# Optimization experiments

Measured on AMD Instinct MI355X. Metric: run time of the kernel, lower is better.

Reference implementation:

```python
import jax, jax.numpy as jnp
import numpy as np

N_WIN = 7  # winsize in PSF.forward
EMBED_DIM = 3
N_EMBED = 8192

def _box_sum(x, n=N_WIN):
    # sliding-window sum with zero padding == torch ZeroPad2d + unfold sum
    C = x.shape[1]
    k = jnp.ones((C, 1, n, n), x.dtype)
    return jax.lax.conv_general_dilated(
        x, k, (1, 1), [(n // 2, n // 2)] * 2,
        feature_group_count=C, dimension_numbers=('NCHW', 'OIHW', 'NCHW'))

def _patch_stats(x, n=N_WIN):
    # mean / unbiased var over the n*n window (zeros included, matching unfold of zero-padded input)
    N = n * n
    s1 = _box_sum(x, n)
    s2 = _box_sum(x * x, n)
    mean = s1 / N
    var = (s2 - s1 * s1 / N) / (N - 1)  # torch .var default unbiased=True
    return mean, var

def _patch_mv_norm(x, n=N_WIN):
    m, v = _patch_stats(x, n)
    return (x - m) / (jnp.sqrt(v) + 1e-8)

def _conv1x1(x, w, b):
    return jnp.einsum('oi,bihw->bohw', w, x) + b[None, :, None, None]

def _ln(x, g, b, eps=1e-5):
    m = x.mean(-1, keepdims=True)
    v = x.var(-1, keepdims=True)
    return (x - m) / jnp.sqrt(v + eps) * g + b

def _mlp(x, w1, b1, w2, b2):
    h = jax.nn.gelu(x @ w1.T + b1, approximate=True)  # GELU(approximate='tanh')
    return h @ w2.T + b2

def _psf(front, back, e_w, e_b, f_w, f_b, g_w, g_b, h_w, h_b):
    x_norm = _patch_mv_norm(front)
    y_mean, y_var = _patch_stats(back)
    x_adain = x_norm * jnp.sqrt(y_var) + y_mean  # patch_adain (no eps on y_std)
    EE = _conv1x1(x_adain, e_w, e_b)
    FF = _conv1x1(_patch_mv_norm(front), f_w, f_b)
    GG = _conv1x1(_patch_mv_norm(back), g_w, g_b)
    HH = _conv1x1(back, h_w, h_b)
    b, c, h, w = GG.shape
    FFf = FF.reshape(b, c, h * w)
    GGf = GG.reshape(b, c, h * w)
    F_n = jnp.sqrt((FFf * FFf).sum(1))
    G_n = jnp.sqrt((GGf * GGf).sum(1))
    S = (FFf * GGf).sum(1) / (F_n * G_n)          # [b, h*w] cosine similarity
    S_min = S.min(1, keepdims=True)
    S_max = S.max(1, keepdims=True)
    S_n = ((S - S_min) / (S_max - S_min)).reshape(b, 1, h, w)
    return S_n * EE + (1 - S_n) * HH

def reference(front, back, mask, bg_embed,
              mi_w1, mi_b1, mi_w2, mi_b2,
              q_w, k_w, v_w,
              mo_w1, mo_b1, mo_w2, mo_b2,
              n1_g, n1_b, n2_g, n2_b,
              e_w, e_b, f_w, f_b, g_w, g_b, h_w, h_b,
              fuse_w, fuse_b):
    fused = _psf(front, back, e_w, e_b, f_w, f_b, g_w, g_b, h_w, h_b)  # [B,3,H,W]
    B, C, H, W = front.shape
    x = front.reshape(B, C, H * W).transpose(0, 2, 1)   # [B, HW, 3] pixel tokens
    x = _mlp(x, mi_w1, mi_b1, mi_w2, mi_b2)             # mlp_in: 3 -> 6 -> embed_dim
    x = _ln(x, n1_g, n1_b)                              # norm1
    ctx = bg_embed.T                                    # [n_embed, embed_dim] codebook as context
    q = x @ q_w.T                                       # [B, HW, d]
    k = ctx @ k_w.T                                     # [n_embed, d]
    v = ctx @ v_w.T                                     # [n_embed, d]
    scale = q.shape[-1] ** (-0.5)
    attn = jax.nn.softmax(jnp.einsum('bld,nd->bln', q, k) * scale, axis=-1)
    x = jnp.einsum('bln,nd->bld', attn, v)              # [B, HW, d]
    x = _mlp(x, mo_w1, mo_b1, mo_w2, mo_b2)             # mlp_out: d -> 6 -> 3
    x = _ln(x, n2_g, n2_b)                              # norm2
    attn_img = x.transpose(0, 2, 1).reshape(B, 3, H, W)
    out = _conv1x1(jnp.concatenate([attn_img, fused], 1), fuse_w, fuse_b)  # fuse: 6 -> 3
    return out

def setup_inputs() -> dict:
    key = jax.random.key(0)
    ks = jax.random.split(key, 32)
    B, H, W = 2, 96, 96
    d = EMBED_DIM
    n = lambda k, s: jax.random.normal(k, s, dtype=jnp.float32)
    inp = {
        'front': n(ks[0], (B, 3, H, W)),
        'back':  n(ks[1], (B, 3, H, W)),
        'mask':  jax.random.uniform(ks[2], (B, 1, H, W), dtype=jnp.float32),
        'bg_embed': n(ks[3], (d, N_EMBED)),
        'mi_w1': n(ks[4], (6, 3)) * 0.5, 'mi_b1': jnp.zeros((6,)),
        'mi_w2': n(ks[5], (d, 6)) * 0.5, 'mi_b2': jnp.zeros((d,)),
        'q_w': n(ks[6], (d, d)) * 0.5,
        'k_w': n(ks[7], (d, d)) * 0.5,
        'v_w': n(ks[8], (d, d)) * 0.5,
        'mo_w1': n(ks[9], (6, d)) * 0.5, 'mo_b1': jnp.zeros((6,)),
        'mo_w2': n(ks[10], (3, 6)) * 0.5, 'mo_b2': jnp.zeros((3,)),
        'n1_g': jnp.ones((d,)), 'n1_b': jnp.zeros((d,)),
        'n2_g': jnp.ones((3,)), 'n2_b': jnp.zeros((3,)),
        'e_w': n(ks[11], (3, 3)) * 0.3, 'e_b': jnp.zeros((3,)),
        'f_w': n(ks[12], (3, 3)) * 0.3, 'f_b': jnp.zeros((3,)),
        'g_w': n(ks[13], (3, 3)) * 0.3, 'g_b': jnp.zeros((3,)),
        'h_w': n(ks[14], (3, 3)) * 0.3, 'h_b': jnp.zeros((3,)),
        'fuse_w': n(ks[15], (3, 6)) * 0.3, 'fuse_b': jnp.zeros((3,)),
    }
    return inp
```

## Files before the change

### kernel.cpp

```cpp
#include <hip/hip_runtime.h>
#include <math.h>

#define HW    9216
#define NPIX  18432
#define NKEY  8192

#define OFF_QPK  0
#define OFF_KPK  (OFF_QPK + NPIX*8)
#define OFF_VT   (OFF_KPK + NKEY*8)
#define OFF_EEHS (OFF_VT + NKEY*4)
#define OFF_MM   (OFF_EEHS + NPIX*8)
#define OFF_PART (OFF_MM + 576)

#if __has_builtin(__builtin_amdgcn_exp2f)
#define EXP2(x) __builtin_amdgcn_exp2f(x)
#else
#define EXP2(x) exp2f(x)
#endif

typedef float f32x4 __attribute__((ext_vector_type(4)));
typedef short bf16x8 __attribute__((ext_vector_type(8)));
typedef unsigned u32x4 __attribute__((ext_vector_type(4)));

__device__ __forceinline__ unsigned bf16rne(float x){
    unsigned b = __builtin_bit_cast(unsigned, x);
    return (b + 0x7FFFu + ((b >> 16) & 1u)) >> 16;
}
__device__ __forceinline__ float bf16tof(unsigned h){
    return __builtin_bit_cast(float, h << 16);
}

__device__ __forceinline__ float gelu_tanh(float x){
    float u = 0.7978845608028654f*(x + 0.044715f*x*x*x);
    return 0.5f*x*(1.0f + tanhf(u));
}

__global__ __launch_bounds__(256) void k1_prep(
    const float* __restrict__ front, const float* __restrict__ back,
    const float* __restrict__ bg,
    const float* __restrict__ k_w,  const float* __restrict__ v_w,
    const float* __restrict__ mi_w1, const float* __restrict__ mi_b1,
    const float* __restrict__ mi_w2, const float* __restrict__ mi_b2,
    const float* __restrict__ q_w,
    const float* __restrict__ n1_g, const float* __restrict__ n1_b,
    const float* __restrict__ e_w,  const float* __restrict__ e_b,
    const float* __restrict__ f_w,  const float* __restrict__ f_b,
    const float* __restrict__ g_w,  const float* __restrict__ g_b,
    const float* __restrict__ h_w,  const float* __restrict__ h_b,
    float* __restrict__ ws)
{
    float* ws_qpk  = ws + OFF_QPK;
    float* ws_kpk  = ws + OFF_KPK;
    float* ws_eehs = ws + OFF_EEHS;
    float* ws_mm   = ws + OFF_MM;

    __shared__ float lds[6][196];
    __shared__ float red[12][256];

    int tid = threadIdx.x;
    int bid = blockIdx.x;
    int img = bid / 144;
    int t   = bid % 144;
    int ty  = (t / 12) * 8;
    int tx  = (t % 12) * 8;

    if (bid < 32){
        int key = bid*256 + tid;
        float c0=bg[key], c1=bg[NKEY+key], c2=bg[2*NKEY+key];
        float kv3[3], vv3[3];
        #pragma unroll
        for (int i=0;i<3;i++){
            kv3[i] = k_w[i*3+0]*c0 + k_w[i*3+1]*c1 + k_w[i*3+2]*c2;
            vv3[i] = v_w[i*3+0]*c0 + v_w[i*3+1]*c1 + v_w[i*3+2]*c2;
        }
        unsigned kh[3], kl[3];
        #pragma unroll
        for (int i=0;i<3;i++){
            kh[i] = bf16rne(kv3[i]);
            kl[i] = bf16rne(kv3[i] - bf16tof(kh[i]));
        }
        unsigned u[8];
        u[0] = kh[0] | (kh[1]<<16);
        u[1] = kh[2] | (kl[0]<<16);
        u[2] = kl[1] | (kl[2]<<16);
        u[3] = kh[0] | (kh[1]<<16);
        u[4] = kh[2]; u[5]=0; u[6]=0; u[7]=0;
        f32x4* kp4 = (f32x4*)ws_kpk;
        kp4[(size_t)key*2+0] = __builtin_bit_cast(f32x4, *(const u32x4*)&u[0]);
        kp4[(size_t)key*2+1] = __builtin_bit_cast(f32x4, *(const u32x4*)&u[4]);
        ((f32x4*)(ws + OFF_VT))[key] = (f32x4){vv3[0], vv3[1], vv3[2], 0.0f};
    }

    const float* fbase = front + img*3*HW;
    const float* bbase = back  + img*3*HW;

    for (int i = tid; i < 196; i += 256){
        int hy = i / 14, hx = i - hy*14;
        int gy = ty + hy - 3, gx = tx + hx - 3;
        bool ok = ((unsigned)gy < 96u) && ((unsigned)gx < 96u);
        int off = gy*96 + gx;
        #pragma unroll
        for (int c=0;c<3;c++){
            lds[c  ][i] = ok ? fbase[c*HW+off] : 0.0f;
            lds[3+c][i] = ok ? bbase[c*HW+off] : 0.0f;
        }
    }
    __syncthreads();

    int p  = tid & 63;
    int qd = tid >> 6;
    int ly = p >> 3, lx = p & 7;

    {
        float s1f[3]={0,0,0}, s2f[3]={0,0,0}, s1b[3]={0,0,0}, s2b[3]={0,0,0};
        int r0 = qd*2;
        int nr = (qd < 3) ? 2 : 1;
        for (int rr=0; rr<nr; ++rr){
            int rb = (ly + r0 + rr)*14 + lx;
            #pragma unroll
            for (int dx=0; dx<7; ++dx){
                #pragma unroll
                for (int c=0;c<3;c++){
                    float fv = lds[c  ][rb+dx];
                    float bv = lds[3+c][rb+dx];
                    s1f[c]+=fv; s2f[c]+=fv*fv;
                    s1b[c]+=bv; s2b[c]+=bv*bv;
                }
            }
        }
        #pragma unroll
        for (int c=0;c<3;c++){
            red[c  ][tid] = s1f[c];
            red[3+c][tid] = s2f[c];
            red[6+c][tid] = s1b[c];
            red[9+c][tid] = s2b[c];
        }
    }
    __syncthreads();

    if (tid < 64){
        float s1f[3]={0,0,0}, s2f[3]={0,0,0}, s1b[3]={0,0,0}, s2b[3]={0,0,0};
        #pragma unroll
        for (int q2=0; q2<4; ++q2){
            int src = p + q2*64;
            #pragma unroll
            for (int c=0;c<3;c++){
                s1f[c] += red[c  ][src];
                s2f[c] += red[3+c][src];
                s1b[c] += red[6+c][src];
                s2b[c] += red[9+c][src];
            }
        }

        int ctr = (ly+3)*14 + (lx+3);
        int pos = (ty+ly)*96 + (tx+lx);
        int pix = img*HW + pos;

        float xnf[3], adain[3], bn[3], bval[3], fctr[3];
        #pragma unroll
        for (int c=0;c<3;c++){
            float mf = s1f[c]*(1.0f/49.0f);
            float vf = (s2f[c] - s1f[c]*s1f[c]*(1.0f/49.0f))*(1.0f/48.0f);
            float fv = lds[c][ctr];
            fctr[c] = fv;
            xnf[c] = (fv - mf)/(sqrtf(vf)+1e-8f);

            float mb = s1b[c]*(1.0f/49.0f);
            float vb = (s2b[c] - s1b[c]*s1b[c]*(1.0f/49.0f))*(1.0f/48.0f);
            float bb = lds[3+c][ctr];
            bval[c]  = bb;
            float stdb = sqrtf(vb);
            adain[c] = xnf[c]*stdb + mb;
            bn[c]    = (bb - mb)/(stdb + 1e-8f);
        }

        float EE[3], FF[3], GG[3], HHv[3];
        #pragma unroll
        for (int i=0;i<3;i++){
            EE[i]  = e_w[i*3+0]*adain[0] + e_w[i*3+1]*adain[1] + e_w[i*3+2]*adain[2] + e_b[i];
            FF[i]  = f_w[i*3+0]*xnf[0]   + f_w[i*3+1]*xnf[1]   + f_w[i*3+2]*xnf[2]   + f_b[i];
            GG[i]  = g_w[i*3+0]*bn[0]    + g_w[i*3+1]*bn[1]    + g_w[i*3+2]*bn[2]    + g_b[i];
            HHv[i] = h_w[i*3+0]*bval[0]  + h_w[i*3+1]*bval[1]  + h_w[i*3+2]*bval[2]  + h_b[i];
        }
        float num = FF[0]*GG[0]+FF[1]*GG[1]+FF[2]*GG[2];
        float fn  = sqrtf(FF[0]*FF[0]+FF[1]*FF[1]+FF[2]*FF[2]);
        float gn  = sqrtf(GG[0]*GG[0]+GG[1]*GG[1]+GG[2]*GG[2]);
        float S   = num/(fn*gn);

        float4* eehs4 = (float4*)ws_eehs;
        eehs4[pix*2+0] = make_float4(EE[0],EE[1],EE[2],S);
        eehs4[pix*2+1] = make_float4(HHv[0],HHv[1],HHv[2],0.0f);

        float mn = S, mx = S;
        #pragma unroll
        for (int off=32; off>0; off>>=1){
            mn = fminf(mn, __shfl_xor(mn, off));
            mx = fmaxf(mx, __shfl_xor(mx, off));
        }
        if (p == 0){ ws_mm[bid*2+0]=mn; ws_mm[bid*2+1]=mx; }

        float xt0 = fctr[0], xt1 = fctr[1], xt2 = fctr[2];
        float h6[6];
        #pragma unroll
        for (int i=0;i<6;i++){
            float a = mi_w1[i*3+0]*xt0 + mi_w1[i*3+1]*xt1 + mi_w1[i*3+2]*xt2 + mi_b1[i];
            h6[i] = gelu_tanh(a);
        }
        float x2[3];
        #pragma unroll
        for (int i=0;i<3;i++){
            float a = mi_b2[i];
            #pragma unroll
            for (int k=0;k<6;k++) a += mi_w2[i*6+k]*h6[k];
            x2[i]=a;
        }
        float m  = (x2[0]+x2[1]+x2[2])*(1.0f/3.0f);
        float d0 = x2[0]-m, d1 = x2[1]-m, d2 = x2[2]-m;
        float var = (d0*d0+d1*d1+d2*d2)*(1.0f/3.0f);
        float inv = 1.0f/sqrtf(var+1e-5f);
        float xn0 = d0*inv*n1_g[0]+n1_b[0];
        float xn1 = d1*inv*n1_g[1]+n1_b[1];
        float xn2 = d2*inv*n1_g[2]+n1_b[2];
        const float qs = 0.5773502691896258f * 1.4426950408889634f;
        float qv[3];
        qv[0] = (q_w[0]*xn0 + q_w[1]*xn1 + q_w[2]*xn2)*qs;
        qv[1] = (q_w[3]*xn0 + q_w[4]*xn1 + q_w[5]*xn2)*qs;
        qv[2] = (q_w[6]*xn0 + q_w[7]*xn1 + q_w[8]*xn2)*qs;

        unsigned qh[3], ql[3];
        #pragma unroll
        for (int i=0;i<3;i++){
            qh[i] = bf16rne(qv[i]);
            ql[i] = bf16rne(qv[i] - bf16tof(qh[i]));
        }
        unsigned u[8];
        u[0] = qh[0] | (qh[1]<<16);
        u[1] = qh[2] | (qh[0]<<16);
        u[2] = qh[1] | (qh[2]<<16);
        u[3] = ql[0] | (ql[1]<<16);
        u[4] = ql[2]; u[5]=0; u[6]=0; u[7]=0;
        f32x4* qp4 = (f32x4*)ws_qpk;
        qp4[(size_t)pix*2+0] = __builtin_bit_cast(f32x4, *(const u32x4*)&u[0]);
        qp4[(size_t)pix*2+1] = __builtin_bit_cast(f32x4, *(const u32x4*)&u[4]);
    }
}

#define RED4(vv, mm) { vv.x += __shfl_xor(vv.x,mm); vv.y += __shfl_xor(vv.y,mm); \
                       vv.z += __shfl_xor(vv.z,mm); vv.w += __shfl_xor(vv.w,mm); }

__global__ __launch_bounds__(256) void k2_attn(const float* __restrict__ ws)
{
    const f32x4* qpk = (const f32x4*)(ws + OFF_QPK);
    const f32x4* kpk = (const f32x4*)(ws + OFF_KPK);
    const f32x4* vt  = (const f32x4*)(ws + OFF_VT);
    f32x4* part      = (f32x4*)(ws + OFF_PART);

    __shared__ f32x4 lkp[512];
    __shared__ f32x4 lv[256];

    int tid  = threadIdx.x;
    int bid  = blockIdx.x;
    int kq   = bid & 7;
    int qg   = bid >> 3;
    int wave = tid >> 6, lane = tid & 63;
    int qtile = qg*4 + wave;
    int g = lane >> 4, col = lane & 15;

    bf16x8 afrag = {0,0,0,0,0,0,0,0};
    if (g < 2)
        afrag = __builtin_bit_cast(bf16x8, qpk[(size_t)(qtile*16 + col)*2 + g]);

    f32x4 s_ = {0,0,0,0}, a0_ = {0,0,0,0}, a1_ = {0,0,0,0}, a2_ = {0,0,0,0};

    const f32x4* kpbase = kpk + ((size_t)kq*1024)*2;
    const f32x4* vbase  = vt + kq*1024;

    for (int chunk=0; chunk<4; ++chunk){
        for (int i=tid; i<512; i+=256) lkp[i] = kpbase[chunk*512 + i];
        if (tid < 256)             lv[tid] = vbase[chunk*256 + tid];
        __syncthreads();
        #pragma unroll 4
        for (int st=0; st<16; ++st){
            bf16x8 bfrag = {0,0,0,0,0,0,0,0};
            if (g < 2)
                bfrag = __builtin_bit_cast(bf16x8, lkp[(st*16+col)*2 + g]);
            f32x4 S = __builtin_amdgcn_mfma_f32_16x16x32_bf16(afrag, bfrag, (f32x4){0,0,0,0}, 0, 0, 0);
            f32x4 v = lv[st*16+col];
            f32x4 p;
            p.x = EXP2(S.x); p.y = EXP2(S.y); p.z = EXP2(S.z); p.w = EXP2(S.w);
            s_  += p;
            a0_ += p * v.x;
            a1_ += p * v.y;
            a2_ += p * v.z;
        }
        __syncthreads();
    }

    RED4(s_, 8) RED4(a0_, 8) RED4(a1_, 8) RED4(a2_, 8)
    RED4(s_, 4) RED4(a0_, 4) RED4(a1_, 4) RED4(a2_, 4)
    RED4(s_, 2) RED4(a0_, 2) RED4(a1_, 2) RED4(a2_, 2)
    RED4(s_, 1) RED4(a0_, 1) RED4(a1_, 1) RED4(a2_, 1)

    int qbase = qtile*16 + g*4;
    f32x4* dst = part + (size_t)kq*NPIX + qbase;
    if      (col==0) dst[0] = (f32x4){s_.x, a0_.x, a1_.x, a2_.x};
    else if (col==1) dst[1] = (f32x4){s_.y, a0_.y, a1_.y, a2_.y};
    else if (col==2) dst[2] = (f32x4){s_.z, a0_.z, a1_.z, a2_.z};
    else if (col==3) dst[3] = (f32x4){s_.w, a0_.w, a1_.w, a2_.w};
}

template<int NC_T>
__global__ __launch_bounds__(256) void k3_final(
    const float* __restrict__ ws,
    const float* __restrict__ mo_w1, const float* __restrict__ mo_b1,
    const float* __restrict__ mo_w2, const float* __restrict__ mo_b2,
    const float* __restrict__ n2_g,  const float* __restrict__ n2_b,
    const float* __restrict__ fuse_w,const float* __restrict__ fuse_b,
    float* __restrict__ out)
{
    const float* ws_eehs = ws + OFF_EEHS;
    const float* ws_mm   = ws + OFF_MM;
    const float* ws_part = ws + OFF_PART;

    int tid = threadIdx.x;
    int g   = tid >> 6;
    int lp  = tid & 63;
    int pixbase = blockIdx.x*64;
    int pix = pixbase + lp;
    int b   = (pix >= HW) ? 1 : 0;

    constexpr int CPG = NC_T/4;
    float s=0.0f, a0=0.0f, a1=0.0f, a2=0.0f;
    const f32x4* part4 = (const f32x4*)ws_part;
    #pragma unroll
    for (int c=g*CPG; c<(g+1)*CPG; ++c){
        f32x4 p = part4[(size_t)c*NPIX + pix];
        s+=p.x; a0+=p.y; a1+=p.z; a2+=p.w;
    }
    __shared__ f32x4 red[256];
    red[tid] = (f32x4){s,a0,a1,a2};

    __shared__ float wmn[4], wmx[4];
    float mn = INFINITY, mx = -INFINITY;
    if (tid < 144){
        mn = ws_mm[(b*144+tid)*2+0];
        mx = ws_mm[(b*144+tid)*2+1];
    }
    #pragma unroll
    for (int off=32; off>0; off>>=1){
        mn = fminf(mn, __shfl_xor(mn, off));
        mx = fmaxf(mx, __shfl_xor(mx, off));
    }
    if ((tid & 63) == 0){ wmn[tid>>6]=mn; wmx[tid>>6]=mx; }
    __syncthreads();

    if (tid < 64){
        mn = fminf(fminf(wmn[0],wmn[1]), fminf(wmn[2],wmn[3]));
        mx = fmaxf(fmaxf(wmx[0],wmx[1]), fmaxf(wmx[2],wmx[3]));

        f32x4 p0 = red[tid], p1 = red[64+tid], p2 = red[128+tid], p3 = red[192+tid];
        s  = p0.x+p1.x+p2.x+p3.x;
        a0 = p0.y+p1.y+p2.y+p3.y;
        a1 = p0.z+p1.z+p2.z+p3.z;
        a2 = p0.w+p1.w+p2.w+p3.w;
        float invs = 1.0f/s;
        float xa0 = a0*invs, xa1 = a1*invs, xa2 = a2*invs;

        float h6[6];
        #pragma unroll
        for (int i=0;i<6;i++){
            float a = mo_w1[i*3+0]*xa0 + mo_w1[i*3+1]*xa1 + mo_w1[i*3+2]*xa2 + mo_b1[i];
            h6[i] = gelu_tanh(a);
        }
        float y[3];
        #pragma unroll
        for (int i=0;i<3;i++){
            float a = mo_b2[i];
            #pragma unroll
            for (int k=0;k<6;k++) a += mo_w2[i*6+k]*h6[k];
            y[i]=a;
        }
        float m  = (y[0]+y[1]+y[2])*(1.0f/3.0f);
        float d0 = y[0]-m, d1 = y[1]-m, d2 = y[2]-m;
        float var = (d0*d0+d1*d1+d2*d2)*(1.0f/3.0f);
        float inv = 1.0f/sqrtf(var+1e-5f);
        float t0 = d0*inv*n2_g[0]+n2_b[0];
        float t1 = d1*inv*n2_g[1]+n2_b[1];
        float t2 = d2*inv*n2_g[2]+n2_b[2];

        float4 e  = ((const float4*)ws_eehs)[pix*2+0];
        float4 hh = ((const float4*)ws_eehs)[pix*2+1];
        float Sn = (e.w - mn)/(mx - mn);
        float f0 = Sn*e.x + (1.0f-Sn)*hh.x;
        float f1 = Sn*e.y + (1.0f-Sn)*hh.y;
        float f2 = Sn*e.z + (1.0f-Sn)*hh.z;

        int pos = pix - b*HW;
        #pragma unroll
        for (int o=0;o<3;o++){
            float val = fuse_b[o]
                      + fuse_w[o*6+0]*t0 + fuse_w[o*6+1]*t1 + fuse_w[o*6+2]*t2
                      + fuse_w[o*6+3]*f0 + fuse_w[o*6+4]*f1 + fuse_w[o*6+5]*f2;
            out[(b*3+o)*HW + pos] = val;
        }
    }
}

extern "C" void kernel_launch(void* const* d_in, const int* in_sizes, int n_in,
                              void* d_out, int out_size, void* d_ws, size_t ws_size,
                              hipStream_t stream) {
    const float* front  = (const float*)d_in[0];
    const float* back   = (const float*)d_in[1];
    const float* bg     = (const float*)d_in[3];
    const float* mi_w1  = (const float*)d_in[4];
    const float* mi_b1  = (const float*)d_in[5];
    const float* mi_w2  = (const float*)d_in[6];
    const float* mi_b2  = (const float*)d_in[7];
    const float* q_w    = (const float*)d_in[8];
    const float* k_w    = (const float*)d_in[9];
    const float* v_w    = (const float*)d_in[10];
    const float* mo_w1  = (const float*)d_in[11];
    const float* mo_b1  = (const float*)d_in[12];
    const float* mo_w2  = (const float*)d_in[13];
    const float* mo_b2  = (const float*)d_in[14];
    const float* n1_g   = (const float*)d_in[15];
    const float* n1_b   = (const float*)d_in[16];
    const float* n2_g   = (const float*)d_in[17];
    const float* n2_b   = (const float*)d_in[18];
    const float* e_w    = (const float*)d_in[19];
    const float* e_b    = (const float*)d_in[20];
    const float* f_w    = (const float*)d_in[21];
    const float* f_b    = (const float*)d_in[22];
    const float* g_w    = (const float*)d_in[23];
    const float* g_b    = (const float*)d_in[24];
    const float* h_w    = (const float*)d_in[25];
    const float* h_b    = (const float*)d_in[26];
    const float* fuse_w = (const float*)d_in[27];
    const float* fuse_b = (const float*)d_in[28];

    float* ws  = (float*)d_ws;
    float* out = (float*)d_out;

    k1_prep<<<dim3(288), 256, 0, stream>>>(
        front, back, bg, k_w, v_w, mi_w1, mi_b1, mi_w2, mi_b2, q_w,
        n1_g, n1_b, e_w, e_b, f_w, f_b, g_w, g_b, h_w, h_b, ws);

    k2_attn<<<dim3(2304), 256, 0, stream>>>(ws);

    k3_final<8><<<dim3(NPIX/64), 256, 0, stream>>>(
        ws, mo_w1, mo_b1, mo_w2, mo_b2, n2_g, n2_b, fuse_w, fuse_b, out);
}
```

Baseline: 50.15 us.

## Switch attention scores to 32x32x16 MFMA with 16-way key split

The attention kernel moves from 16x16x32 bf16 MFMA, where half the K dimension was zero padding, to 32x32x16 MFMA so every lane carries useful Q/K fragment data. Each wave now handles 32 queries, and the key range is split 16 ways instead of 8, with 512 keys per block. The final combine kernel is instantiated for 16 partials to match. This uses more accumulator registers (64 floats per lane), a longer 5-step shuffle reduction, and twice as many partials written to and read back from memory.

After: 93.93 us. +87.3%, slower.

```diff
diff --git a/kernel.cpp b/kernel.cpp
--- a/kernel.cpp
+++ b/kernel.cpp
@@ -18,7 +18,8 @@
 #define EXP2(x) exp2f(x)
 #endif
 
-typedef float f32x4 __attribute__((ext_vector_type(4)));
+typedef float f32x4  __attribute__((ext_vector_type(4)));
+typedef float f32x16 __attribute__((ext_vector_type(16)));
 typedef short bf16x8 __attribute__((ext_vector_type(8)));
 typedef unsigned u32x4 __attribute__((ext_vector_type(4)));
 
@@ -245,9 +246,6 @@
     }
 }
 
-#define RED4(vv, mm) { vv.x += __shfl_xor(vv.x,mm); vv.y += __shfl_xor(vv.y,mm); \
-                       vv.z += __shfl_xor(vv.z,mm); vv.w += __shfl_xor(vv.w,mm); }
-
 __global__ __launch_bounds__(256) void k2_attn(const float* __restrict__ ws)
 {
     const f32x4* qpk = (const f32x4*)(ws + OFF_QPK);
@@ -260,53 +258,64 @@
 
     int tid  = threadIdx.x;
     int bid  = blockIdx.x;
-    int kq   = bid & 7;
-    int qg   = bid >> 3;
+    int kq   = bid & 15;
+    int qg   = bid >> 4;
     int wave = tid >> 6, lane = tid & 63;
     int qtile = qg*4 + wave;
-    int g = lane >> 4, col = lane & 15;
-
-    bf16x8 afrag = {0,0,0,0,0,0,0,0};
-    if (g < 2)
-        afrag = __builtin_bit_cast(bf16x8, qpk[(size_t)(qtile*16 + col)*2 + g]);
-
-    f32x4 s_ = {0,0,0,0}, a0_ = {0,0,0,0}, a1_ = {0,0,0,0}, a2_ = {0,0,0,0};
-
-    const f32x4* kpbase = kpk + ((size_t)kq*1024)*2;
-    const f32x4* vbase  = vt + kq*1024;
-
-    for (int chunk=0; chunk<4; ++chunk){
+    int col  = lane & 31;
+    int half = lane >> 5;
+
+    bf16x8 afrag = __builtin_bit_cast(bf16x8, qpk[(size_t)(qtile*32 + col)*2 + half]);
+
+    f32x16 s_  = {0,0,0,0,0,0,0,0,0,0,0,0,0,0,0,0};
+    f32x16 a0_ = {0,0,0,0,0,0,0,0,0,0,0,0,0,0,0,0};
+    f32x16 a1_ = {0,0,0,0,0,0,0,0,0,0,0,0,0,0,0,0};
+    f32x16 a2_ = {0,0,0,0,0,0,0,0,0,0,0,0,0,0,0,0};
+
+    const f32x4* kpbase = kpk + ((size_t)kq*512)*2;
+    const f32x4* vbase  = vt + kq*512;
+
+    for (int chunk=0; chunk<2; ++chunk){
         for (int i=tid; i<512; i+=256) lkp[i] = kpbase[chunk*512 + i];
         if (tid < 256)             lv[tid] = vbase[chunk*256 + tid];
         __syncthreads();
-        #pragma unroll 4
-        for (int st=0; st<16; ++st){
-            bf16x8 bfrag = {0,0,0,0,0,0,0,0};
-            if (g < 2)
-                bfrag = __builtin_bit_cast(bf16x8, lkp[(st*16+col)*2 + g]);
-            f32x4 S = __builtin_amdgcn_mfma_f32_16x16x32_bf16(afrag, bfrag, (f32x4){0,0,0,0}, 0, 0, 0);
-            f32x4 v = lv[st*16+col];
-            f32x4 p;
-            p.x = EXP2(S.x); p.y = EXP2(S.y); p.z = EXP2(S.z); p.w = EXP2(S.w);
-            s_  += p;
-            a0_ += p * v.x;
-            a1_ += p * v.y;
-            a2_ += p * v.z;
+        for (int st=0; st<8; ++st){
+            bf16x8 bfrag = __builtin_bit_cast(bf16x8, lkp[(st*32+col)*2 + half]);
+            f32x4 v = lv[st*32+col];
+            f32x16 S = __builtin_amdgcn_mfma_f32_32x32x16_bf16(afrag, bfrag,
+                        (f32x16){0,0,0,0,0,0,0,0,0,0,0,0,0,0,0,0}, 0, 0, 0);
+            #pragma unroll
+            for (int r=0;r<16;r++){
+                float pp = EXP2(S[r]);
+                s_[r]  += pp;
+                a0_[r] += pp * v.x;
+                a1_[r] += pp * v.y;
+                a2_[r] += pp * v.z;
+            }
         }
         __syncthreads();
     }
 
-    RED4(s_, 8) RED4(a0_, 8) RED4(a1_, 8) RED4(a2_, 8)
-    RED4(s_, 4) RED4(a0_, 4) RED4(a1_, 4) RED4(a2_, 4)
-    RED4(s_, 2) RED4(a0_, 2) RED4(a1_, 2) RED4(a2_, 2)
-    RED4(s_, 1) RED4(a0_, 1) RED4(a1_, 1) RED4(a2_, 1)
-
-    int qbase = qtile*16 + g*4;
-    f32x4* dst = part + (size_t)kq*NPIX + qbase;
-    if      (col==0) dst[0] = (f32x4){s_.x, a0_.x, a1_.x, a2_.x};
-    else if (col==1) dst[1] = (f32x4){s_.y, a0_.y, a1_.y, a2_.y};
-    else if (col==2) dst[2] = (f32x4){s_.z, a0_.z, a1_.z, a2_.z};
-    else if (col==3) dst[3] = (f32x4){s_.w, a0_.w, a1_.w, a2_.w};
+    #pragma unroll
+    for (int mloop=0; mloop<5; ++mloop){
+        int m = 16 >> mloop;
+        #pragma unroll
+        for (int r=0;r<16;r++){
+            s_[r]  += __shfl_xor(s_[r],  m);
+            a0_[r] += __shfl_xor(a0_[r], m);
+            a1_[r] += __shfl_xor(a1_[r], m);
+            a2_[r] += __shfl_xor(a2_[r], m);
+        }
+    }
+
+    if (col == 0){
+        f32x4* dst = part + (size_t)kq*NPIX + qtile*32;
+        #pragma unroll
+        for (int r=0;r<16;r++){
+            int q = (r&3) + 8*(r>>2) + 4*half;
+            dst[q] = (f32x4){s_[r], a0_[r], a1_[r], a2_[r]};
+        }
+    }
 }
 
 template<int NC_T>
@@ -447,6 +456,6 @@
 
     k2_attn<<<dim3(2304), 256, 0, stream>>>(ws);
 
-    k3_final<8><<<dim3(NPIX/64), 256, 0, stream>>>(
+    k3_final<16><<<dim3(NPIX/64), 256, 0, stream>>>(
         ws, mo_w1, mo_b1, mo_w2, mo_b2, n2_g, n2_b, fuse_w, fuse_b, out);
 }
```
